# Optimization experiments

Hardware: AMD Instinct MI355X
Metric: run time of the kernel (lower is better)

The kernel has to match this reference:

```python
import jax, jax.numpy as jnp
import numpy as np
from jax import lax

B, J, I = 32, 48, 48          # batch, target len, source len
W = 2                          # target_window_size
CTX = 2 * W + 1                # 5
E, H = 128, 256                # embedding_size, hidden_units
VT, VS = 32000, 32000          # target / source vocab
S = 2 * J                      # HMM states (word + null)


def setup_inputs() -> dict:
    key = jax.random.key(0)
    ks = jax.random.split(key, 12)
    inp = {
        "target_embedding": jax.random.normal(ks[0], (VT, E), jnp.float32) * 0.02,
        "W_bridge": jax.random.normal(ks[1], (E * CTX, E), jnp.float32) * 0.02,
        "W_hidden": jax.random.normal(ks[2], (E, H), jnp.float32) * 0.02,
        "b_hidden": jnp.zeros((H,), jnp.float32),
        "W_vocab": jax.random.normal(ks[3], (H, VS), jnp.float32) * 0.02,
        "b_vocab": jnp.zeros((VS,), jnp.float32),
        "transition": jax.random.uniform(ks[4], (B, S, S), jnp.float32, 0.01, 1.0),
        "initial_transition": jax.random.uniform(ks[5], (B, S), jnp.float32, 0.01, 1.0),
        "targets_ctx": jax.random.randint(ks[6], (B, J * CTX), 0, VT, jnp.int32),
        "targets_ctx_null": jax.random.randint(ks[7], (B, J * CTX), 0, VT, jnp.int32),
        "sources": jax.random.randint(ks[8], (B, I), 0, VS, jnp.int32),
    }
    return inp


def _emission(emb, Wb, Wh, bh, Wv, bv, ctx_ids, sources):
    # embedding lookup + context reshape: [B, J*CTX, E] -> [B, J, CTX*E]
    x = emb[ctx_ids].reshape(ctx_ids.shape[0], -1, CTX * E)
    h = jnp.tanh(jnp.einsum('bjc,ce,eh->bjh', x, Wb, Wh) + bh)  # bridge+hidden
    probs = jax.nn.softmax(h @ Wv + bv, axis=-1)                # [B, J, VS]
    # per-example gather of source token columns -> [B, J, I]
    return jax.vmap(lambda p, s: p[:, s])(probs, sources)


def _forward_backward(pi, A, em):
    # pi [B,S], A [B,S,S], em [B,S,I]; scaled HMM forward-backward
    e = jnp.moveaxis(em, 2, 0)  # [I, B, S]
    a0 = pi * e[0]
    c0 = a0.sum(-1, keepdims=True)
    a0 = a0 / c0

    def fstep(a, ei):
        an = jnp.einsum('bs,bst->bt', a, A) * ei
        c = an.sum(-1, keepdims=True)
        an = an / c
        return an, (an, c)

    _, (alphas, cs) = lax.scan(fstep, a0, e[1:])
    alphas = jnp.concatenate([a0[None], alphas], 0)          # [I,B,S]
    cs = jnp.concatenate([c0[None], cs], 0)                  # [I,B,1]

    def bstep(b, inp):
        ei, ci = inp
        bn = jnp.einsum('bst,bt->bs', A, ei * b) / ci
        return bn, bn

    bI = jnp.ones_like(a0)
    _, betas_rev = lax.scan(bstep, bI, (e[1:][::-1], cs[1:][::-1]))
    betas = jnp.concatenate([betas_rev[::-1], bI[None]], 0)  # [I,B,S]

    gamma = alphas * betas                                   # state posteriors
    loglik = jnp.log(cs[..., 0]).sum(0)                      # [B]
    return jnp.moveaxis(gamma, 0, 2), loglik


def reference(target_embedding, W_bridge, W_hidden, b_hidden, W_vocab, b_vocab,
              transition, initial_transition, targets_ctx, targets_ctx_null, sources):
    em_word = _emission(target_embedding, W_bridge, W_hidden, b_hidden,
                        W_vocab, b_vocab, targets_ctx, sources)       # [B,J,I]
    em_null = _emission(target_embedding, W_bridge, W_hidden, b_hidden,
                        W_vocab, b_vocab, targets_ctx_null, sources)  # [B,J,I]
    emission = jnp.concatenate([em_word, em_null], axis=1)            # [B,2J,I]
    gamma, loglik = _forward_backward(initial_transition, transition, emission)
    return gamma, -loglik
```

## Files before the change

kernel.cpp:

```cpp
#include <hip/hip_runtime.h>
#include <hip/hip_bf16.h>

#define NB 32
#define NJ 48
#define NI 48
#define NCTX 5
#define NE 128
#define NH 256
#define NVS 32000
#define NS 96
#define NR 3072

typedef __attribute__((ext_vector_type(8))) short bf16x8;
typedef __attribute__((ext_vector_type(4))) float f32x4;

__device__ __forceinline__ unsigned short f2b(float f) {
  __hip_bfloat16 h = __float2bfloat16(f);
  return *reinterpret_cast<unsigned short*>(&h);
}
__device__ __forceinline__ float wave_sum(float v) {
  v += __shfl_xor(v, 1);
  v += __shfl_xor(v, 2);
  v += __shfl_xor(v, 4);
  v += __shfl_xor(v, 8);
  v += __shfl_xor(v, 16);
  v += __shfl_xor(v, 32);
  return v;
}
__device__ __forceinline__ void gload_lds16(const void* g, void* l) {
  __builtin_amdgcn_global_load_lds(
      (const __attribute__((address_space(1))) void*)g,
      (__attribute__((address_space(3))) void*)l, 16, 0, 0);
}


__global__ __launch_bounds__(256) void k_transpose(const float* __restrict__ Wv,
                                                   unsigned char* __restrict__ Wv8) {
  __shared__ float tile[64][65];
  int t = threadIdx.x;
  int v0 = blockIdx.x * 64, k0 = blockIdx.y * 64;
  {
    int kr = t >> 4, vq = t & 15;
#pragma unroll
    for (int it = 0; it < 4; ++it) {
      float4 v = *(const float4*)&Wv[(k0 + kr + 16 * it) * NVS + v0 + vq * 4];
      tile[kr + 16 * it][vq * 4 + 0] = v.x;
      tile[kr + 16 * it][vq * 4 + 1] = v.y;
      tile[kr + 16 * it][vq * 4 + 2] = v.z;
      tile[kr + 16 * it][vq * 4 + 3] = v.w;
    }
  }
  __syncthreads();
  {
    int vl = t >> 2, kq = t & 3;
    unsigned int q8[4];
#pragma unroll
    for (int d = 0; d < 4; ++d) {
      float f0 = tile[kq * 16 + d * 4 + 0][vl] * 64.0f;
      float f1 = tile[kq * 16 + d * 4 + 1][vl] * 64.0f;
      float f2 = tile[kq * 16 + d * 4 + 2][vl] * 64.0f;
      float f3 = tile[kq * 16 + d * 4 + 3][vl] * 64.0f;
      int w = __builtin_amdgcn_cvt_pk_fp8_f32(f0, f1, 0, false);
      w = __builtin_amdgcn_cvt_pk_fp8_f32(f2, f3, w, true);
      q8[d] = (unsigned int)w;
    }
    int kqp = kq ^ ((vl >> 2) & 3);
    unsigned int q8s[4];
    if ((vl >> 1) & 1) {
      q8s[0] = q8[2]; q8s[1] = q8[3]; q8s[2] = q8[0]; q8s[3] = q8[1];
    } else {
      q8s[0] = q8[0]; q8s[1] = q8[1]; q8s[2] = q8[2]; q8s[3] = q8[3];
    }
    *(uint4*)&Wv8[(v0 + vl) * 256 + k0 + kqp * 16] = *(uint4*)q8s;
  }
}

__global__ __launch_bounds__(256) void k_t2b(const float* __restrict__ src,
                                             unsigned short* __restrict__ dst,
                                             int R, int C) {
  __shared__ float tile[64][65];
  int t = threadIdx.x;
  int r0 = blockIdx.x * 64, c0 = blockIdx.y * 64;
  {
    int rr = t >> 4, cq = t & 15;
#pragma unroll
    for (int it = 0; it < 4; ++it) {
      float4 v = *(const float4*)&src[(r0 + rr + 16 * it) * C + c0 + cq * 4];
      tile[rr + 16 * it][cq * 4 + 0] = v.x;
      tile[rr + 16 * it][cq * 4 + 1] = v.y;
      tile[rr + 16 * it][cq * 4 + 2] = v.z;
      tile[rr + 16 * it][cq * 4 + 3] = v.w;
    }
  }
  __syncthreads();
  {
    int cc = t >> 2, rq = t & 3;
    unsigned short pk[16];
#pragma unroll
    for (int q = 0; q < 16; ++q) pk[q] = f2b(tile[rq * 16 + q][cc]);
    *(uint4*)&dst[(c0 + cc) * R + r0 + rq * 16] = *(uint4*)&pk[0];
    *(uint4*)&dst[(c0 + cc) * R + r0 + rq * 16 + 8] = *(uint4*)&pk[8];
  }
}

__global__ __launch_bounds__(256) void k_xb(const float* __restrict__ emb,
                                            const unsigned short* __restrict__ Wbt,
                                            const int* __restrict__ tc, const int* __restrict__ tcn,
                                            unsigned short* __restrict__ xb) {
  __shared__ unsigned short Ax[32 * 72];
  __shared__ unsigned short Bw[128 * 72];
  __shared__ unsigned short xout[32 * 136];
  int t = threadIdx.x;
  int r0 = blockIdx.x * 32;
  int wave = t >> 6, lane = t & 63;
  int wm = wave >> 1, wn = wave & 1;
  int lg = lane >> 4, lr = lane & 15;
  int arow = t >> 3, aseg = t & 7;
  int r = r0 + arow;
  int half = r / 1536, rem = r % 1536, bb = rem / 48, jj = rem % 48;
  const int* ids = half ? tcn : tc;
  int brow = t >> 1, bseg = t & 1;

  f32x4 acc[4];
#pragma unroll
  for (int n = 0; n < 4; ++n) acc[n] = (f32x4){0.f, 0.f, 0.f, 0.f};

  for (int step = 0; step < 10; ++step) {
    int k0 = step * 64;
    int p = step >> 1;
    int e0 = (step & 1) * 64;
    {
      int id = ids[bb * 240 + jj * 5 + p];
      const float4* er = (const float4*)&emb[id * 128 + e0 + aseg * 8];
      float4 v0 = er[0], v1 = er[1];
      unsigned short pk[8];
      pk[0] = f2b(v0.x); pk[1] = f2b(v0.y); pk[2] = f2b(v0.z); pk[3] = f2b(v0.w);
      pk[4] = f2b(v1.x); pk[5] = f2b(v1.y); pk[6] = f2b(v1.z); pk[7] = f2b(v1.w);
      *(uint4*)&Ax[arow * 72 + aseg * 8] = *(uint4*)&pk[0];
    }
    {
      const uint4* wp = (const uint4*)&Wbt[brow * 640 + k0 + bseg * 32];
      uint4* dp = (uint4*)&Bw[brow * 72 + bseg * 32];
      uint4 w0 = wp[0], w1 = wp[1], w2 = wp[2], w3 = wp[3];
      dp[0] = w0; dp[1] = w1; dp[2] = w2; dp[3] = w3;
    }
    __syncthreads();
#pragma unroll
    for (int kk = 0; kk < 2; ++kk) {
      bf16x8 a = *(const bf16x8*)&Ax[(wm * 16 + lr) * 72 + kk * 32 + lg * 8];
#pragma unroll
      for (int n = 0; n < 4; ++n) {
        bf16x8 b = *(const bf16x8*)&Bw[(wn * 64 + n * 16 + lr) * 72 + kk * 32 + lg * 8];
        acc[n] = __builtin_amdgcn_mfma_f32_16x16x32_bf16(a, b, acc[n], 0, 0, 0);
      }
    }
    __syncthreads();
  }
#pragma unroll
  for (int n = 0; n < 4; ++n)
#pragma unroll
    for (int g = 0; g < 4; ++g)
      xout[(wm * 16 + lg * 4 + g) * 136 + wn * 64 + n * 16 + lr] = f2b(acc[n][g]);
  __syncthreads();
  {
    int orow = t >> 3, os = t & 7;
    *(uint4*)&xb[(r0 + orow) * 128 + os * 16] = *(uint4*)&xout[orow * 136 + os * 16];
    *(uint4*)&xb[(r0 + orow) * 128 + os * 16 + 8] = *(uint4*)&xout[orow * 136 + os * 16 + 8];
  }
}

__global__ __launch_bounds__(256) void k_h(const unsigned short* __restrict__ xb,
                                           const unsigned short* __restrict__ Wht,
                                           const float* __restrict__ bh,
                                           unsigned char* __restrict__ hb8) {
  __shared__ char smem[69632];
  unsigned short* Asm = (unsigned short*)smem;
  unsigned short* Bsm = (unsigned short*)(smem + 34816);
  unsigned char* o8 = (unsigned char*)smem;
  int t = threadIdx.x;
  int r0 = blockIdx.x * 128, n0 = blockIdx.y * 128;
  int wave = t >> 6, lane = t & 63;
  int wm = wave >> 1, wn = wave & 1;
  int lg = lane >> 4, lr = lane & 15;
  {
    int row = t >> 1, seg = t & 1;
#pragma unroll
    for (int i = 0; i < 8; ++i) {
      *(uint4*)&Asm[row * 136 + seg * 64 + i * 8] = *(const uint4*)&xb[(r0 + row) * 128 + seg * 64 + i * 8];
      *(uint4*)&Bsm[row * 136 + seg * 64 + i * 8] = *(const uint4*)&Wht[(n0 + row) * 128 + seg * 64 + i * 8];
    }
  }
  __syncthreads();
  f32x4 acc[4][4];
#pragma unroll
  for (int m = 0; m < 4; ++m)
#pragma unroll
    for (int n = 0; n < 4; ++n) acc[m][n] = (f32x4){0.f, 0.f, 0.f, 0.f};
#pragma unroll
  for (int kk = 0; kk < 4; ++kk) {
    bf16x8 a[4], b[4];
#pragma unroll
    for (int m = 0; m < 4; ++m)
      a[m] = *(const bf16x8*)&Asm[(wm * 64 + m * 16 + lr) * 136 + kk * 32 + lg * 8];
#pragma unroll
    for (int n = 0; n < 4; ++n)
      b[n] = *(const bf16x8*)&Bsm[(wn * 64 + n * 16 + lr) * 136 + kk * 32 + lg * 8];
#pragma unroll
    for (int m = 0; m < 4; ++m)
#pragma unroll
      for (int n = 0; n < 4; ++n)
        acc[m][n] = __builtin_amdgcn_mfma_f32_16x16x32_bf16(a[m], b[n], acc[m][n], 0, 0, 0);
  }
  __syncthreads();
#pragma unroll
  for (int n = 0; n < 4; ++n) {
    int cl = wn * 64 + n * 16 + lr;
    float bvv = bh[n0 + cl];
#pragma unroll
    for (int m = 0; m < 4; ++m) {
#pragma unroll
      for (int g = 0; g < 4; ++g) {
        int rl = wm * 64 + m * 16 + lg * 4 + g;
        float hv = tanhf(acc[m][n][g] + bvv);
        int p8 = __builtin_amdgcn_cvt_pk_fp8_f32(hv * 256.0f, 0.0f, 0, false);
        o8[rl * 144 + cl] = (unsigned char)(p8 & 0xFF);
      }
    }
  }
  __syncthreads();
  {
    int row = t >> 1, seg = t & 1;
    int sig = (row >> 1) & 7;
    int swp = row & 1;
#pragma unroll
    for (int i = 0; i < 4; ++i) {
      int p_loc = seg * 4 + i;
      int w_loc = p_loc ^ sig;
      unsigned long long q[2];
      q[0] = *(const unsigned long long*)&o8[row * 144 + w_loc * 16 + swp * 8];
      q[1] = *(const unsigned long long*)&o8[row * 144 + w_loc * 16 + (swp ^ 1) * 8];
      *(uint4*)&hb8[(r0 + row) * 256 + n0 + p_loc * 16] = *(uint4*)q;
    }
  }
}

__global__ __launch_bounds__(256) void k_denom(const unsigned char* __restrict__ hb8,
                                               const unsigned char* __restrict__ Wv8,
                                               const float* __restrict__ bv,
                                               float* __restrict__ dpart) {
  __shared__ __align__(16) unsigned char smem[49152];
  unsigned char* Asm = smem;
  float* red2 = (float*)smem;
  unsigned char* bufp[2] = {smem + 32768, smem + 40960};
  int t = threadIdx.x;
  int bid = blockIdx.x;
  int xcd = bid & 7;
  int pos = bid >> 3;
  int tile = xcd * 375 + pos;
  int vtp = tile / 24, rt = tile % 24;
  int r0 = rt * 128;
  int wave = t >> 6, lane = t & 63;
  int wm = wave >> 1, wn = wave & 1;
  int lg = lane >> 4, lr = lane & 15;

#pragma unroll
  for (int c = 0; c < 8; ++c) {
    int inst = wave * 8 + c;
    gload_lds16(&hb8[(r0 + inst * 4 + (lane >> 4)) * 256 + (lane & 15) * 16], &Asm[inst * 1024]);
  }
#pragma unroll
  for (int c = 0; c < 2; ++c) {
    int i = wave * 2 + c;
    gload_lds16(&Wv8[(vtp * 256 + i * 16 + (lane >> 2)) * 256 + 0 * 64 + (lane & 3) * 16],
                bufp[0] + i * 1024);
  }
  __syncthreads();

  long long a_reg[4][8];
#pragma unroll
  for (int m = 0; m < 4; ++m) {
    int rowb = (wm * 64 + m * 16 + lr) * 256;
#pragma unroll
    for (int ks = 0; ks < 4; ++ks)
#pragma unroll
      for (int kk = 0; kk < 2; ++kk)
        a_reg[m][ks * 2 + kk] =
            *(const long long*)&Asm[rowb + (((ks * 8 + kk * 4 + lg) ^ lr) << 3)];
  }

  const float SC = 6.103515625e-05f;
  f32x4 acc[4][4];
#pragma unroll
  for (int m = 0; m < 4; ++m)
#pragma unroll
    for (int n = 0; n < 4; ++n) acc[m][n] = (f32x4){0.f, 0.f, 0.f, 0.f};

#pragma unroll
  for (int step = 0; step < 8; ++step) {
    int vt = step >> 2, ks = step & 3, buf = step & 1;
    if (step < 7) {
      int ns = step + 1;
      int nvt = ns >> 2, nks = ns & 3;
      int vb2 = (vtp * 2 + nvt) * 128;
#pragma unroll
      for (int c = 0; c < 2; ++c) {
        int i = wave * 2 + c;
        gload_lds16(&Wv8[(vb2 + i * 16 + (lane >> 2)) * 256 + nks * 64 + (lane & 3) * 16],
                    bufp[buf ^ 1] + i * 1024);
      }
    }
#pragma unroll
    for (int kk = 0; kk < 2; ++kk) {
      long long b[4];
#pragma unroll
      for (int n = 0; n < 4; ++n) {
        int rr = wn * 64 + n * 16 + lr;
        b[n] = *(const long long*)&bufp[buf][rr * 64 + (((kk * 4 + lg) ^ ((rr >> 1) & 7)) << 3)];
      }
      __builtin_amdgcn_s_setprio(1);
#pragma unroll
      for (int m = 0; m < 4; ++m)
#pragma unroll
        for (int n = 0; n < 4; ++n)
          acc[m][n] = __builtin_amdgcn_mfma_f32_16x16x32_fp8_fp8(a_reg[m][ks * 2 + kk], b[n],
                                                                 acc[m][n], 0, 0, 0);
      __builtin_amdgcn_s_setprio(0);
    }
    if (ks == 3) {
      int v0 = (vtp * 2 + vt) * 128;
      float rs[4][4];
#pragma unroll
      for (int m = 0; m < 4; ++m)
#pragma unroll
        for (int g = 0; g < 4; ++g) rs[m][g] = 0.f;
#pragma unroll
      for (int m = 0; m < 4; ++m) {
#pragma unroll
        for (int n = 0; n < 4; ++n) {
          float bvv = bv[v0 + wn * 64 + n * 16 + lr];
#pragma unroll
          for (int g = 0; g < 4; ++g) rs[m][g] += __expf(acc[m][n][g] * SC + bvv);
          acc[m][n] = (f32x4){0.f, 0.f, 0.f, 0.f};
        }
      }
#pragma unroll
      for (int m = 0; m < 4; ++m)
#pragma unroll
        for (int g = 0; g < 4; ++g) {
          float v = rs[m][g];
          v += __shfl_xor(v, 1);
          v += __shfl_xor(v, 2);
          v += __shfl_xor(v, 4);
          v += __shfl_xor(v, 8);
          rs[m][g] = v;
        }
      if (lr == 0) {
#pragma unroll
        for (int m = 0; m < 4; ++m)
#pragma unroll
          for (int g = 0; g < 4; ++g)
            red2[wn * 128 + wm * 64 + m * 16 + lg * 4 + g] = rs[m][g];
      }
      __syncthreads();
      if (t < 128) dpart[(vtp * 2 + vt) * NR + r0 + t] = red2[t] + red2[128 + t];
    } else {
      __syncthreads();
    }
  }
}

__global__ void k_reduce(const float* __restrict__ dpart, float* __restrict__ dsum) {
  int r = blockIdx.x * 256 + threadIdx.x;
  float s = 0.f;
  for (int vt = 0; vt < 250; ++vt) s += dpart[vt * NR + r];
  dsum[r] = s;
}

__global__ __launch_bounds__(64) void k_emis(const unsigned char* __restrict__ hb8,
                                             const unsigned char* __restrict__ Wv8,
                                             const float* __restrict__ bv,
                                             const float* __restrict__ dsum,
                                             const int* __restrict__ src,
                                             float* __restrict__ em) {
  __shared__ unsigned char A8[48 * 256];
  __shared__ unsigned char B8[48 * 256];
  __shared__ int s_src[48];
  int t = threadIdx.x;
  int bh = blockIdx.x;
  int b = bh & 31, half = bh >> 5;
  int row4 = t >> 4, seg = t & 15;
  int rbase = half * 1536 + b * 48;
  if (t < 48) s_src[t] = src[b * 48 + t];
#pragma unroll
  for (int c = 0; c < 12; ++c) {
    int row = c * 4 + row4;
    gload_lds16(&hb8[(rbase + row) * 256 + seg * 16], &A8[c * 1024]);
    int sv = src[b * 48 + row];
    gload_lds16(&Wv8[sv * 256 + seg * 16], &B8[c * 1024]);
  }
  __syncthreads();
  int lg = t >> 4, lr = t & 15;
  int svr[3];
#pragma unroll
  for (int m = 0; m < 3; ++m) svr[m] = s_src[m * 16 + lr];
  f32x4 acc[3][3];
#pragma unroll
  for (int m = 0; m < 3; ++m)
#pragma unroll
    for (int n = 0; n < 3; ++n) acc[m][n] = (f32x4){0.f, 0.f, 0.f, 0.f};
#pragma unroll
  for (int kk = 0; kk < 8; ++kk) {
    int sa = kk * 4 + lg;
    long long a[3], bb[3];
#pragma unroll
    for (int m = 0; m < 3; ++m) {
      int rr = m * 16 + lr;
      a[m] = *(const long long*)&A8[rr * 256 + ((sa ^ lr) << 3)];
      bb[m] = *(const long long*)&B8[rr * 256 + ((sa >> 3) << 6) +
                                     (((sa & 7) ^ ((svr[m] >> 1) & 7)) << 3)];
    }
#pragma unroll
    for (int m = 0; m < 3; ++m)
#pragma unroll
      for (int n = 0; n < 3; ++n)
        acc[m][n] = __builtin_amdgcn_mfma_f32_16x16x32_fp8_fp8(a[m], bb[n], acc[m][n], 0, 0, 0);
  }
  const float SC = 6.103515625e-05f;
#pragma unroll
  for (int n = 0; n < 3; ++n) {
    int i = n * 16 + lr;
    float bvv = bv[svr[n]];
#pragma unroll
    for (int m = 0; m < 3; ++m) {
#pragma unroll
      for (int g = 0; g < 4; ++g) {
        int j = m * 16 + lg * 4 + g;
        float val = __expf(acc[m][n][g] * SC + bvv) / dsum[rbase + j];
        em[b * 4608 + (half * 48 + j) * 48 + i] = val;
      }
    }
  }
}

__global__ __launch_bounds__(192) void k_fb(const float* __restrict__ Atr, const float* __restrict__ pi,
                                            const float* __restrict__ em, float* __restrict__ alph,
                                            float* __restrict__ betas, float* __restrict__ out1) {
  __shared__ float A_st[96 * 97];
  __shared__ float em_lds[48 * 97];
  __shared__ __align__(16) float vec_lds[96];
  __shared__ float red[3];
  int t = threadIdx.x;
  int bid = blockIdx.x;
  int b = bid & 31;
  int role = bid >> 5;
  int col = t >> 1, half = t & 1;
  int base = b * 4608;

  for (int idx = t; idx < 96 * 96; idx += 192) {
    int s = idx / 96, tt = idx % 96;
    A_st[s * 97 + tt] = Atr[b * 9216 + idx];
  }
  for (int idx = t; idx < 96 * 48; idx += 192) {
    int s = idx / 48, i = idx % 48;
    em_lds[i * 97 + s] = em[base + idx];
  }
  __syncthreads();

  float Areg[48];
  if (role == 0) {
#pragma unroll
    for (int ss = 0; ss < 48; ++ss) Areg[ss] = A_st[(half * 48 + ss) * 97 + col];

    float llsum;
    {
      float v = pi[b * 96 + col] * em_lds[0 * 97 + col];
      float ws = half ? 0.f : v;
      ws = wave_sum(ws);
      if ((t & 63) == 0) red[t >> 6] = ws;
      __syncthreads();
      float c = red[0] + red[1] + red[2];
      float a = v / c;
      if (!half) {
        vec_lds[col] = a;
        alph[base + col] = a;
      }
      llsum = logf(c);
      __syncthreads();
    }
    for (int i = 1; i < 48; ++i) {
      float p = 0.f;
      const float4* ap = (const float4*)&vec_lds[half * 48];
#pragma unroll
      for (int q = 0; q < 12; ++q) {
        float4 av = ap[q];
        p += av.x * Areg[4 * q] + av.y * Areg[4 * q + 1] + av.z * Areg[4 * q + 2] + av.w * Areg[4 * q + 3];
      }
      p += __shfl_xor(p, 1);
      float an = p * em_lds[i * 97 + col];
      float ws = half ? 0.f : an;
      ws = wave_sum(ws);
      if ((t & 63) == 0) red[t >> 6] = ws;
      __syncthreads();
      float c = red[0] + red[1] + red[2];
      float a = an / c;
      if (!half) {
        vec_lds[col] = a;
        alph[base + i * 96 + col] = a;
      }
      llsum += logf(c);
      __syncthreads();
    }
    if (t == 0) out1[b] = -llsum;
  } else {
#pragma unroll
    for (int tt = 0; tt < 48; ++tt) Areg[tt] = A_st[col * 97 + half * 48 + tt];

    if (!half) {
      betas[base + 47 * 96 + col] = 1.0f;
      vec_lds[col] = em_lds[47 * 97 + col];
    }
    __syncthreads();
    for (int i = 46; i >= 0; --i) {
      float p = 0.f;
      const float4* ep = (const float4*)&vec_lds[half * 48];
#pragma unroll
      for (int q = 0; q < 12; ++q) {
        float4 ev = ep[q];
        p += ev.x * Areg[4 * q] + ev.y * Areg[4 * q + 1] + ev.z * Areg[4 * q + 2] + ev.w * Areg[4 * q + 3];
      }
      p += __shfl_xor(p, 1);
      float ws = half ? 0.f : p;
      ws = wave_sum(ws);
      if ((t & 63) == 0) red[t >> 6] = ws;
      __syncthreads();
      float c = red[0] + red[1] + red[2];
      float bt = p / c;
      if (!half) {
        betas[base + i * 96 + col] = bt;
        vec_lds[col] = em_lds[i * 97 + col] * bt;
      }
      __syncthreads();
    }
  }
}

__global__ __launch_bounds__(128) void k_gamma(const float* __restrict__ alph,
                                               const float* __restrict__ betas,
                                               float* __restrict__ out0) {
  __shared__ float red[2];
  int b = blockIdx.x, i = blockIdx.y;
  int t = threadIdx.x;
  float g = 0.f;
  if (t < 96) g = alph[b * 4608 + i * 96 + t] * betas[b * 4608 + i * 96 + t];
  float ws = wave_sum(g);
  if ((t & 63) == 0) red[t >> 6] = ws;
  __syncthreads();
  float c = red[0] + red[1];
  if (t < 96) out0[b * 4608 + t * 48 + i] = g / c;
}

extern "C" void kernel_launch(void* const* d_in, const int* in_sizes, int n_in,
                              void* d_out, int out_size, void* d_ws, size_t ws_size,
                              hipStream_t stream) {
  const float* emb = (const float*)d_in[0];
  const float* Wb  = (const float*)d_in[1];
  const float* Wh  = (const float*)d_in[2];
  const float* bh  = (const float*)d_in[3];
  const float* Wv  = (const float*)d_in[4];
  const float* bv  = (const float*)d_in[5];
  const float* Atr = (const float*)d_in[6];
  const float* pi  = (const float*)d_in[7];
  const int* tc    = (const int*)d_in[8];
  const int* tcn   = (const int*)d_in[9];
  const int* src   = (const int*)d_in[10];

  float* out0 = (float*)d_out;
  float* out1 = out0 + NB * NS * NI;

  char* ws = (char*)d_ws;
  unsigned char* wv8 = (unsigned char*)(ws);
  unsigned char* hb8 = (unsigned char*)(ws + 8192000);
  float* dpart       = (float*)(ws + 8978432);
  float* betas       = (float*)(ws + 8978432);
  float* dsum        = (float*)(ws + 12050432);
  float* em          = (float*)(ws + 12062720);
  float* alph        = (float*)(ws + 12652544);
  unsigned short* wbt = (unsigned short*)(ws + 13242368);
  unsigned short* wht = (unsigned short*)(ws + 13406208);
  unsigned short* xb  = (unsigned short*)(ws + 13471744);

  k_transpose<<<dim3(500, 4), 256, 0, stream>>>(Wv, wv8);
  k_t2b<<<dim3(10, 2), 256, 0, stream>>>(Wb, wbt, 640, 128);
  k_t2b<<<dim3(2, 4), 256, 0, stream>>>(Wh, wht, 128, 256);
  k_xb<<<96, 256, 0, stream>>>(emb, wbt, tc, tcn, xb);
  k_h<<<dim3(24, 2), 256, 0, stream>>>(xb, wht, bh, hb8);
  k_denom<<<3000, 256, 0, stream>>>(hb8, wv8, bv, dpart);
  k_reduce<<<12, 256, 0, stream>>>(dpart, dsum);
  k_emis<<<64, 64, 0, stream>>>(hb8, wv8, bv, dsum, src, em);
  k_fb<<<64, 192, 0, stream>>>(Atr, pi, em, alph, betas, out1);
  k_gamma<<<dim3(32, 48), 128, 0, stream>>>(alph, betas, out0);
}
```

Measured before the change: 150.3 us.

## Load vocab weights directly from global in denominator GEMM, drop LDS staging and barriers

The denominator kernel no longer stages Wv8 tiles through double-buffered LDS with per-step barriers. Each wave now reads its B fragments straight from global memory, relying on the pre-swizzled layout. Per-wave partial sums are written directly to dpart, which doubles the number of partials, so k_reduce loops over 500 slices and the workspace offsets are shifted. This removes LDS traffic, __syncthreads and a shared reduction, and shrinks LDS use so more blocks can be resident. In exchange it loses the explicit prefetch overlap, puts global latency on the MFMA path, and doubles the reduction reads.

```diff
diff --git a/kernel.cpp b/kernel.cpp
--- a/kernel.cpp
+++ b/kernel.cpp
@@ -248,10 +248,7 @@
                                                const unsigned char* __restrict__ Wv8,
                                                const float* __restrict__ bv,
                                                float* __restrict__ dpart) {
-  __shared__ __align__(16) unsigned char smem[49152];
-  unsigned char* Asm = smem;
-  float* red2 = (float*)smem;
-  unsigned char* bufp[2] = {smem + 32768, smem + 40960};
+  __shared__ __align__(16) unsigned char Asm[32768];
   int t = threadIdx.x;
   int bid = blockIdx.x;
   int xcd = bid & 7;
@@ -268,12 +265,6 @@
     int inst = wave * 8 + c;
     gload_lds16(&hb8[(r0 + inst * 4 + (lane >> 4)) * 256 + (lane & 15) * 16], &Asm[inst * 1024]);
   }
-#pragma unroll
-  for (int c = 0; c < 2; ++c) {
-    int i = wave * 2 + c;
-    gload_lds16(&Wv8[(vtp * 256 + i * 16 + (lane >> 2)) * 256 + 0 * 64 + (lane & 3) * 16],
-                bufp[0] + i * 1024);
-  }
   __syncthreads();
 
   long long a_reg[4][8];
@@ -281,90 +272,74 @@
   for (int m = 0; m < 4; ++m) {
     int rowb = (wm * 64 + m * 16 + lr) * 256;
 #pragma unroll
-    for (int ks = 0; ks < 4; ++ks)
-#pragma unroll
-      for (int kk = 0; kk < 2; ++kk)
-        a_reg[m][ks * 2 + kk] =
-            *(const long long*)&Asm[rowb + (((ks * 8 + kk * 4 + lg) ^ lr) << 3)];
+    for (int s = 0; s < 8; ++s)
+      a_reg[m][s] = *(const long long*)&Asm[rowb + (((s * 4 + lg) ^ lr) << 3)];
   }
 
   const float SC = 6.103515625e-05f;
-  f32x4 acc[4][4];
-#pragma unroll
-  for (int m = 0; m < 4; ++m)
-#pragma unroll
-    for (int n = 0; n < 4; ++n) acc[m][n] = (f32x4){0.f, 0.f, 0.f, 0.f};
-
-#pragma unroll
-  for (int step = 0; step < 8; ++step) {
-    int vt = step >> 2, ks = step & 3, buf = step & 1;
-    if (step < 7) {
-      int ns = step + 1;
-      int nvt = ns >> 2, nks = ns & 3;
-      int vb2 = (vtp * 2 + nvt) * 128;
-#pragma unroll
-      for (int c = 0; c < 2; ++c) {
-        int i = wave * 2 + c;
-        gload_lds16(&Wv8[(vb2 + i * 16 + (lane >> 2)) * 256 + nks * 64 + (lane & 3) * 16],
-                    bufp[buf ^ 1] + i * 1024);
-      }
-    }
-#pragma unroll
-    for (int kk = 0; kk < 2; ++kk) {
-      long long b[4];
+  int sg = (lr >> 1) & 7;
+
+#pragma unroll
+  for (int vt = 0; vt < 2; ++vt) {
+    const unsigned char* Bp = Wv8 + ((size_t)((vtp * 2 + vt) * 128 + wn * 64 + lr)) * 256;
+    f32x4 acc[4][4];
+#pragma unroll
+    for (int m = 0; m < 4; ++m)
+#pragma unroll
+      for (int n = 0; n < 4; ++n) acc[m][n] = (f32x4){0.f, 0.f, 0.f, 0.f};
+
+#pragma unroll
+    for (int ks = 0; ks < 4; ++ks) {
+#pragma unroll
+      for (int kk = 0; kk < 2; ++kk) {
+        int so = ks * 64 + ((((kk << 2) + lg) ^ sg) << 3);
+        long long b[4];
+#pragma unroll
+        for (int n = 0; n < 4; ++n)
+          b[n] = *(const long long*)(Bp + n * 4096 + so);
+        __builtin_amdgcn_s_setprio(1);
+#pragma unroll
+        for (int m = 0; m < 4; ++m)
+#pragma unroll
+          for (int n = 0; n < 4; ++n)
+            acc[m][n] = __builtin_amdgcn_mfma_f32_16x16x32_fp8_fp8(a_reg[m][ks * 2 + kk], b[n],
+                                                                   acc[m][n], 0, 0, 0);
+        __builtin_amdgcn_s_setprio(0);
+      }
+    }
+    int v0 = (vtp * 2 + vt) * 128;
+    float rs[4][4];
+#pragma unroll
+    for (int m = 0; m < 4; ++m)
+#pragma unroll
+      for (int g = 0; g < 4; ++g) rs[m][g] = 0.f;
+#pragma unroll
+    for (int m = 0; m < 4; ++m) {
 #pragma unroll
       for (int n = 0; n < 4; ++n) {
-        int rr = wn * 64 + n * 16 + lr;
-        b[n] = *(const long long*)&bufp[buf][rr * 64 + (((kk * 4 + lg) ^ ((rr >> 1) & 7)) << 3)];
-      }
-      __builtin_amdgcn_s_setprio(1);
+        float bvv = bv[v0 + wn * 64 + n * 16 + lr];
+#pragma unroll
+        for (int g = 0; g < 4; ++g) rs[m][g] += __expf(acc[m][n][g] * SC + bvv);
+      }
+    }
+#pragma unroll
+    for (int m = 0; m < 4; ++m)
+#pragma unroll
+      for (int g = 0; g < 4; ++g) {
+        float v = rs[m][g];
+        v += __shfl_xor(v, 1);
+        v += __shfl_xor(v, 2);
+        v += __shfl_xor(v, 4);
+        v += __shfl_xor(v, 8);
+        rs[m][g] = v;
+      }
+    if (lr == 0) {
+      int d = (vtp * 2 + vt) * 2 + wn;
 #pragma unroll
       for (int m = 0; m < 4; ++m)
 #pragma unroll
-        for (int n = 0; n < 4; ++n)
-          acc[m][n] = __builtin_amdgcn_mfma_f32_16x16x32_fp8_fp8(a_reg[m][ks * 2 + kk], b[n],
-                                                                 acc[m][n], 0, 0, 0);
-      __builtin_amdgcn_s_setprio(0);
-    }
-    if (ks == 3) {
-      int v0 = (vtp * 2 + vt) * 128;
-      float rs[4][4];
-#pragma unroll
-      for (int m = 0; m < 4; ++m)
-#pragma unroll
-        for (int g = 0; g < 4; ++g) rs[m][g] = 0.f;
-#pragma unroll
-      for (int m = 0; m < 4; ++m) {
-#pragma unroll
-        for (int n = 0; n < 4; ++n) {
-          float bvv = bv[v0 + wn * 64 + n * 16 + lr];
-#pragma unroll
-          for (int g = 0; g < 4; ++g) rs[m][g] += __expf(acc[m][n][g] * SC + bvv);
-          acc[m][n] = (f32x4){0.f, 0.f, 0.f, 0.f};
-        }
-      }
-#pragma unroll
-      for (int m = 0; m < 4; ++m)
-#pragma unroll
-        for (int g = 0; g < 4; ++g) {
-          float v = rs[m][g];
-          v += __shfl_xor(v, 1);
-          v += __shfl_xor(v, 2);
-          v += __shfl_xor(v, 4);
-          v += __shfl_xor(v, 8);
-          rs[m][g] = v;
-        }
-      if (lr == 0) {
-#pragma unroll
-        for (int m = 0; m < 4; ++m)
-#pragma unroll
-          for (int g = 0; g < 4; ++g)
-            red2[wn * 128 + wm * 64 + m * 16 + lg * 4 + g] = rs[m][g];
-      }
-      __syncthreads();
-      if (t < 128) dpart[(vtp * 2 + vt) * NR + r0 + t] = red2[t] + red2[128 + t];
-    } else {
-      __syncthreads();
+        for (int g = 0; g < 4; ++g)
+          dpart[d * NR + r0 + wm * 64 + m * 16 + lg * 4 + g] = rs[m][g];
     }
   }
 }
@@ -372,7 +347,7 @@
 __global__ void k_reduce(const float* __restrict__ dpart, float* __restrict__ dsum) {
   int r = blockIdx.x * 256 + threadIdx.x;
   float s = 0.f;
-  for (int vt = 0; vt < 250; ++vt) s += dpart[vt * NR + r];
+  for (int vt = 0; vt < 500; ++vt) s += dpart[vt * NR + r];
   dsum[r] = s;
 }
 
@@ -582,12 +557,12 @@
   unsigned char* hb8 = (unsigned char*)(ws + 8192000);
   float* dpart       = (float*)(ws + 8978432);
   float* betas       = (float*)(ws + 8978432);
-  float* dsum        = (float*)(ws + 12050432);
-  float* em          = (float*)(ws + 12062720);
-  float* alph        = (float*)(ws + 12652544);
-  unsigned short* wbt = (unsigned short*)(ws + 13242368);
-  unsigned short* wht = (unsigned short*)(ws + 13406208);
-  unsigned short* xb  = (unsigned short*)(ws + 13471744);
+  float* dsum        = (float*)(ws + 15122432);
+  float* em          = (float*)(ws + 15134720);
+  float* alph        = (float*)(ws + 15724544);
+  unsigned short* wbt = (unsigned short*)(ws + 16314368);
+  unsigned short* wht = (unsigned short*)(ws + 16478208);
+  unsigned short* xb  = (unsigned short*)(ws + 16543744);
 
   k_transpose<<<dim3(500, 4), 256, 0, stream>>>(Wv, wv8);
   k_t2b<<<dim3(10, 2), 256, 0, stream>>>(Wb, wbt, 640, 128);
```

Result: slower. 168.8 us (+12.3%).
